# Optimization experiments

Hardware: AMD Instinct MI355X
Metric: run time of the kernel (lower is better)

Reference implementation:

```python
import jax, jax.numpy as jnp
import numpy as np

B, T, C = 2, 4096, 1024
H = 16
D = C // H  # head_dim = 64


def setup_inputs() -> dict:
    key = jax.random.key(0)
    k1, k2, k3 = jax.random.split(key, 3)
    x = jax.random.normal(k1, (B, T, C), dtype=jnp.float32)
    W_qkv = jax.random.normal(k2, (3 * C, C), dtype=jnp.float32) * (1.0 / np.sqrt(C))
    W_out = jax.random.normal(k3, (C, C), dtype=jnp.float32) * (1.0 / np.sqrt(C))
    return {"x": x, "W_qkv": W_qkv, "W_out": W_out}


def reference(x, W_qkv, W_out):
    b, t, c = x.shape
    # qkv projection: torch Linear y = x @ W.T  -> (B,T,3C)
    qkv = jnp.einsum('btc,fc->btf', x, W_qkv)
    qkv = qkv.reshape(b, t, 3, H, D)
    q, k, v = qkv[:, :, 0], qkv[:, :, 1], qkv[:, :, 2]  # (B,T,H,D)
    q = q.transpose(0, 2, 1, 3)  # (B,H,T,D)
    k = k.transpose(0, 2, 1, 3)
    v = v.transpose(0, 2, 1, 3)
    scale = 1.0 / np.sqrt(D).astype(np.float32)
    att = jnp.einsum('bhqd,bhkd->bhqk', q, k) * scale  # (B,H,T,T)
    causal = jnp.tril(jnp.ones((t, t), dtype=bool))
    att = jnp.where(causal[None, None], att, jnp.float32(-jnp.inf))
    att = jax.nn.softmax(att, axis=-1)
    # dropout p=0.0 -> identity
    out = jnp.einsum('bhqk,bhkd->bhqd', att, v)  # (B,H,T,D)
    out = out.transpose(0, 2, 1, 3).reshape(b, t, c)
    return jnp.einsum('btc,oc->bto', out, W_out)
```

## Files before the change

### kernel.cpp

```cpp
#include <hip/hip_runtime.h>

constexpr int Bn = 2;
constexpr int Tn = 4096;
constexpr int Cn = 1024;
constexpr int Hn = 16;
constexpr int Dn = 64;

typedef __bf16 bf16x8 __attribute__((ext_vector_type(8)));
typedef float f32x4 __attribute__((ext_vector_type(4)));
typedef unsigned short u16x8 __attribute__((ext_vector_type(8)));

__device__ __forceinline__ unsigned short f2bf(float f) {
  unsigned int u = __float_as_uint(f);
  u += 0x7FFF + ((u >> 16) & 1);
  return (unsigned short)(u >> 16);
}

__device__ __forceinline__ bf16x8 ld_bf8(const unsigned short* p) {
  return __builtin_bit_cast(bf16x8, *(const u16x8*)p);
}

__global__ void cvt_kernel(const float* __restrict__ in, unsigned short* __restrict__ out, int n4) {
  int i = blockIdx.x * blockDim.x + threadIdx.x;
  if (i >= n4) return;
  float4 v = ((const float4*)in)[i];
  ushort4 o;
  o.x = f2bf(v.x); o.y = f2bf(v.y); o.z = f2bf(v.z); o.w = f2bf(v.w);
  ((ushort4*)out)[i] = o;
}

template<int OUT_BF16>
__global__ __launch_bounds__(256) void gemm_bt(const unsigned short* __restrict__ A,
                                               const unsigned short* __restrict__ Bm,
                                               void* __restrict__ Cout,
                                               int M, int N, int K) {
  __shared__ __align__(16) unsigned short As[128][64];
  __shared__ __align__(16) unsigned short Bs[128][64];
  const int tid  = threadIdx.x;
  const int wave = tid >> 6;
  const int lane = tid & 63;
  const int wr   = (wave >> 1) * 64;
  const int wc   = (wave & 1) * 64;
  const int lrow = lane & 15;
  const int lk8  = (lane >> 4) << 3;
  const int row0 = blockIdx.y * 128;
  const int col0 = blockIdx.x * 128;

  f32x4 acc[4][4];
  #pragma unroll
  for (int i = 0; i < 4; ++i)
    #pragma unroll
    for (int j = 0; j < 4; ++j)
      acc[i][j] = (f32x4){0.f, 0.f, 0.f, 0.f};

  for (int k0 = 0; k0 < K; k0 += 64) {
    const unsigned short* Ag = A  + (size_t)row0 * K + k0;
    const unsigned short* Bg = Bm + (size_t)col0 * K + k0;
    #pragma unroll
    for (int i = 0; i < 4; ++i) {
      int flat = (i * 256 + tid) * 8;
      int r = flat >> 6, c = flat & 63;
      __builtin_amdgcn_global_load_lds((const __attribute__((address_space(1))) void*)(Ag + (size_t)r * K + c),
                                       (__attribute__((address_space(3))) void*)(&As[r][c]), 16, 0, 0);
    }
    #pragma unroll
    for (int i = 0; i < 4; ++i) {
      int flat = (i * 256 + tid) * 8;
      int r = flat >> 6, c = flat & 63;
      __builtin_amdgcn_global_load_lds((const __attribute__((address_space(1))) void*)(Bg + (size_t)r * K + c),
                                       (__attribute__((address_space(3))) void*)(&Bs[r][c]), 16, 0, 0);
    }
    __syncthreads();

    #pragma unroll
    for (int ks = 0; ks < 2; ++ks) {
      bf16x8 af[4], bfr[4];
      #pragma unroll
      for (int i = 0; i < 4; ++i) af[i]  = ld_bf8(&As[wr + i * 16 + lrow][ks * 32 + lk8]);
      #pragma unroll
      for (int j = 0; j < 4; ++j) bfr[j] = ld_bf8(&Bs[wc + j * 16 + lrow][ks * 32 + lk8]);
      #pragma unroll
      for (int i = 0; i < 4; ++i)
        #pragma unroll
        for (int j = 0; j < 4; ++j)
          acc[i][j] = __builtin_amdgcn_mfma_f32_16x16x32_bf16(af[i], bfr[j], acc[i][j], 0, 0, 0);
    }
    __syncthreads();
  }

  const int rg = (lane >> 4) * 4;
  const int cl = lane & 15;
  #pragma unroll
  for (int i = 0; i < 4; ++i)
    #pragma unroll
    for (int j = 0; j < 4; ++j)
      #pragma unroll
      for (int rr = 0; rr < 4; ++rr) {
        int gm = row0 + wr + i * 16 + rg + rr;
        int gn = col0 + wc + j * 16 + cl;
        float v = acc[i][j][rr];
        if (OUT_BF16) ((unsigned short*)Cout)[(size_t)gm * N + gn] = f2bf(v);
        else          ((float*)Cout)[(size_t)gm * N + gn] = v;
      }
}

__global__ __launch_bounds__(256) void vtrans_kernel(const unsigned short* __restrict__ qkv,
                                                     unsigned short* __restrict__ vT) {
  __shared__ __align__(16) unsigned short L[64 * 64];
  const int tid = threadIdx.x;
  const int t0  = blockIdx.x * 64;
  const int bh  = blockIdx.y;
  const int b   = bh >> 4;
  const int h   = bh & 15;
  const unsigned short* src = qkv + (size_t)b * Tn * (3 * Cn) + 2 * Cn + h * Dn;

  #pragma unroll
  for (int i = 0; i < 2; ++i) {
    int flat = i * 256 + tid;
    int t = flat >> 3, c = flat & 7;
    int cs = c ^ ((t >> 3) & 7);
    __builtin_amdgcn_global_load_lds(
        (const __attribute__((address_space(1))) void*)(src + (size_t)(t0 + t) * (3 * Cn) + cs * 8),
        (__attribute__((address_space(3))) void*)(&L[flat * 8]), 16, 0, 0);
  }
  __syncthreads();

  #pragma unroll
  for (int i = 0; i < 2; ++i) {
    int flat = i * 256 + tid;
    int d = flat >> 3, tc = flat & 7;
    u16x8 o;
    #pragma unroll
    for (int j = 0; j < 8; ++j) {
      int t = tc * 8 + j;
      o[j] = L[t * 64 + (((d >> 3) ^ ((t >> 3) & 7)) << 3) + (d & 7)];
    }
    *(u16x8*)(vT + ((size_t)bh * 64 + d) * Tn + t0 + tc * 8) = o;
  }
}

__global__ __launch_bounds__(256) void attn_kernel(const unsigned short* __restrict__ qkv,
                                                   const unsigned short* __restrict__ vT,
                                                   unsigned short* __restrict__ outb) {
  __shared__ __align__(16) unsigned short Ks[2][4096];
  __shared__ __align__(16) unsigned short Vs[2][4096];
  __shared__ __align__(16) unsigned short Ps[4][1024];

  const int tid  = threadIdx.x;
  const int wave = tid >> 6;
  const int lane = tid & 63;
  const int cl   = lane & 15;
  const int g    = lane >> 4;
  const int lk8  = g << 3;
  const int rg   = g * 4;

  const int orig = blockIdx.y * gridDim.x + blockIdx.x;
  const int cid  = (orig & 7) * 256 + (orig >> 3);
  const int qt   = (63 - (cid & 63)) * 64;
  const int bh   = cid >> 6;
  const int b    = bh >> 4;
  const int h    = bh & 15;

  const unsigned short* qb  = qkv + (size_t)b * Tn * (3 * Cn) + h * Dn;
  const unsigned short* kb  = qb + Cn;
  const unsigned short* vtb = vT + (size_t)bh * Dn * Tn;

  bf16x8 qf[2];
  {
    const unsigned short* qr = qb + (size_t)(qt + wave * 16 + cl) * (3 * Cn) + lk8;
    qf[0] = ld_bf8(qr);
    qf[1] = ld_bf8(qr + 32);
    #pragma unroll
    for (int j = 0; j < 8; ++j) {
      qf[0][j] = qf[0][j] * (__bf16)0.125f;
      qf[1][j] = qf[1][j] * (__bf16)0.125f;
    }
  }

  f32x4 oacc[4];
  #pragma unroll
  for (int n = 0; n < 4; ++n) oacc[n] = (f32x4){0.f, 0.f, 0.f, 0.f};
  float mrun[4] = {-1e30f, -1e30f, -1e30f, -1e30f};
  float lrun[4] = {0.f, 0.f, 0.f, 0.f};

  #pragma unroll
  for (int i = 0; i < 2; ++i) {
    const int flat = i * 256 + tid;
    const int r    = flat >> 3;
    const int cg   = flat & 7;
    const int sw   = cg ^ (r & 7);
    __builtin_amdgcn_global_load_lds(
        (const __attribute__((address_space(1))) void*)(kb + (size_t)r * (3 * Cn) + sw * 8),
        (__attribute__((address_space(3))) void*)(&Ks[0][flat * 8]), 16, 0, 0);
    __builtin_amdgcn_global_load_lds(
        (const __attribute__((address_space(1))) void*)(vtb + (size_t)r * Tn + sw * 8),
        (__attribute__((address_space(3))) void*)(&Vs[0][flat * 8]), 16, 0, 0);
  }
  __syncthreads();

  const int nkv = qt / 64 + 1;
  for (int kt = 0; kt < nkv; ++kt) {
    const int kv0 = kt * 64;
    const int cur = kt & 1;
    const int nb  = cur ^ 1;
    const bool pre = (kt + 1 < nkv);

    if (pre) {
      const int kv1 = kv0 + 64;
      #pragma unroll
      for (int i = 0; i < 2; ++i) {
        const int flat = i * 256 + tid;
        const int r    = flat >> 3;
        const int cg   = flat & 7;
        const int sw   = cg ^ (r & 7);
        __builtin_amdgcn_global_load_lds(
            (const __attribute__((address_space(1))) void*)(kb + (size_t)(kv1 + r) * (3 * Cn) + sw * 8),
            (__attribute__((address_space(3))) void*)(&Ks[nb][flat * 8]), 16, 0, 0);
        __builtin_amdgcn_global_load_lds(
            (const __attribute__((address_space(1))) void*)(vtb + (size_t)r * Tn + kv1 + sw * 8),
            (__attribute__((address_space(3))) void*)(&Vs[nb][flat * 8]), 16, 0, 0);
      }
    }

    f32x4 s[4];
    #pragma unroll
    for (int n = 0; n < 4; ++n) s[n] = (f32x4){0.f, 0.f, 0.f, 0.f};
    __builtin_amdgcn_s_setprio(1);
    #pragma unroll
    for (int n = 0; n < 4; ++n)
      #pragma unroll
      for (int ks = 0; ks < 2; ++ks) {
        bf16x8 kf = ld_bf8(&Ks[cur][(n * 16 + cl) * 64 + (((ks * 4 + g) ^ (cl & 7)) << 3)]);
        s[n] = __builtin_amdgcn_mfma_f32_16x16x32_bf16(qf[ks], kf, s[n], 0, 0, 0);
      }
    __builtin_amdgcn_s_setprio(0);

    const bool diag = (kv0 == qt);
    if (diag) {
      #pragma unroll
      for (int n = 0; n < 4; ++n)
        #pragma unroll
        for (int rr = 0; rr < 4; ++rr) {
          int ql = wave * 16 + rg + rr;
          int kl = n * 16 + cl;
          if (kl > ql) s[n][rr] = -1e30f;
        }
    }

    #pragma unroll
    for (int rr = 0; rr < 4; ++rr) {
      float mx = fmaxf(fmaxf(s[0][rr], s[1][rr]), fmaxf(s[2][rr], s[3][rr]));
      mx = fmaxf(mx, __shfl_xor(mx, 1));
      mx = fmaxf(mx, __shfl_xor(mx, 2));
      mx = fmaxf(mx, __shfl_xor(mx, 4));
      mx = fmaxf(mx, __shfl_xor(mx, 8));
      float mnew  = fmaxf(mrun[rr], mx);
      float alpha = __expf(mrun[rr] - mnew);
      mrun[rr] = mnew;
      float sum = 0.f;
      #pragma unroll
      for (int n = 0; n < 4; ++n) {
        float p = __expf(s[n][rr] - mnew);
        s[n][rr] = p;
        sum += p;
      }
      sum += __shfl_xor(sum, 1);
      sum += __shfl_xor(sum, 2);
      sum += __shfl_xor(sum, 4);
      sum += __shfl_xor(sum, 8);
      lrun[rr] = lrun[rr] * alpha + sum;
      #pragma unroll
      for (int n = 0; n < 4; ++n) oacc[n][rr] *= alpha;
    }

    #pragma unroll
    for (int n = 0; n < 4; ++n)
      #pragma unroll
      for (int rr = 0; rr < 4; ++rr) {
        const int row  = rg + rr;
        const int slot = n * 2 + (cl >> 3);
        Ps[wave][row * 64 + ((slot ^ (row & 7)) << 3) + (cl & 7)] = f2bf(s[n][rr]);
      }

    #pragma unroll
    for (int ks = 0; ks < 2; ++ks) {
      bf16x8 pa = ld_bf8(&Ps[wave][cl * 64 + (((ks * 4 + g) ^ (cl & 7)) << 3)]);
      __builtin_amdgcn_s_setprio(1);
      #pragma unroll
      for (int n = 0; n < 4; ++n) {
        bf16x8 vf = ld_bf8(&Vs[cur][(n * 16 + cl) * 64 + (((ks * 4 + g) ^ (cl & 7)) << 3)]);
        oacc[n] = __builtin_amdgcn_mfma_f32_16x16x32_bf16(pa, vf, oacc[n], 0, 0, 0);
      }
      __builtin_amdgcn_s_setprio(0);
    }

    __syncthreads();
  }

  #pragma unroll
  for (int rr = 0; rr < 4; ++rr) {
    float inv = 1.0f / lrun[rr];
    int t = qt + wave * 16 + rg + rr;
    size_t rowo = ((size_t)b * Tn + t) * Cn + h * Dn;
    #pragma unroll
    for (int n = 0; n < 4; ++n)
      outb[rowo + n * 16 + cl] = f2bf(oacc[n][rr] * inv);
  }
}

extern "C" void kernel_launch(void* const* d_in, const int* in_sizes, int n_in,
                              void* d_out, int out_size, void* d_ws, size_t ws_size,
                              hipStream_t stream) {
  const float* x    = (const float*)d_in[0];
  const float* Wqkv = (const float*)d_in[1];
  const float* Wout = (const float*)d_in[2];
  float* y = (float*)d_out;

  unsigned short* xb    = (unsigned short*)d_ws;
  unsigned short* wqkvb = xb    + (size_t)Bn * Tn * Cn;
  unsigned short* woutb = wqkvb + (size_t)3 * Cn * Cn;
  unsigned short* qkvb  = woutb + (size_t)Cn * Cn;
  unsigned short* attno = qkvb  + (size_t)Bn * Tn * 3 * Cn;

  const int M = Bn * Tn;

  {
    int n4 = (Bn * Tn * Cn) / 4;
    cvt_kernel<<<(n4 + 255) / 256, 256, 0, stream>>>(x, xb, n4);
  }
  {
    int n4 = (3 * Cn * Cn) / 4;
    cvt_kernel<<<(n4 + 255) / 256, 256, 0, stream>>>(Wqkv, wqkvb, n4);
  }
  {
    int n4 = (Cn * Cn) / 4;
    cvt_kernel<<<(n4 + 255) / 256, 256, 0, stream>>>(Wout, woutb, n4);
  }

  gemm_bt<1><<<dim3(3 * Cn / 128, M / 128), 256, 0, stream>>>(xb, wqkvb, qkvb, M, 3 * Cn, Cn);

  unsigned short* vT = xb;
  vtrans_kernel<<<dim3(Tn / 64, Bn * Hn), 256, 0, stream>>>(qkvb, vT);

  attn_kernel<<<dim3(Tn / 64, Bn * Hn), 256, 0, stream>>>(qkvb, vT, attno);

  gemm_bt<0><<<dim3(Cn / 128, M / 128), 256, 0, stream>>>(attno, woutb, y, M, Cn, Cn);

  (void)in_sizes; (void)n_in; (void)out_size; (void)ws_size;
}
```

Measured before the change: 448.6 us.

## Skip softmax rescale when max unchanged, defer row-sum reduce, swizzle GEMM tiles

New measurement: 413.0 us. 1.09x faster.

```diff
diff --git a/kernel.cpp b/kernel.cpp
--- a/kernel.cpp
+++ b/kernel.cpp
@@ -14,6 +14,10 @@
   unsigned int u = __float_as_uint(f);
   u += 0x7FFF + ((u >> 16) & 1);
   return (unsigned short)(u >> 16);
+}
+
+__device__ __forceinline__ unsigned short f2bf_hw(float f) {
+  return __builtin_bit_cast(unsigned short, (__bf16)f);
 }
 
 __device__ __forceinline__ bf16x8 ld_bf8(const unsigned short* p) {
@@ -43,8 +47,13 @@
   const int wc   = (wave & 1) * 64;
   const int lrow = lane & 15;
   const int lk8  = (lane >> 4) << 3;
-  const int row0 = blockIdx.y * 128;
-  const int col0 = blockIdx.x * 128;
+
+  const int nbx  = gridDim.x;
+  const int nwg  = nbx * gridDim.y;
+  const int orig = blockIdx.y * nbx + blockIdx.x;
+  const int cid  = (orig & 7) * (nwg >> 3) + (orig >> 3);
+  const int row0 = (cid / nbx) * 128;
+  const int col0 = (cid % nbx) * 128;
 
   f32x4 acc[4][4];
   #pragma unroll
@@ -247,6 +256,7 @@
         }
     }
 
+    float pmax[4];
     #pragma unroll
     for (int rr = 0; rr < 4; ++rr) {
       float mx = fmaxf(fmaxf(s[0][rr], s[1][rr]), fmaxf(s[2][rr], s[3][rr]));
@@ -254,23 +264,39 @@
       mx = fmaxf(mx, __shfl_xor(mx, 2));
       mx = fmaxf(mx, __shfl_xor(mx, 4));
       mx = fmaxf(mx, __shfl_xor(mx, 8));
-      float mnew  = fmaxf(mrun[rr], mx);
-      float alpha = __expf(mrun[rr] - mnew);
-      mrun[rr] = mnew;
-      float sum = 0.f;
-      #pragma unroll
-      for (int n = 0; n < 4; ++n) {
-        float p = __expf(s[n][rr] - mnew);
-        s[n][rr] = p;
-        sum += p;
-      }
-      sum += __shfl_xor(sum, 1);
-      sum += __shfl_xor(sum, 2);
-      sum += __shfl_xor(sum, 4);
-      sum += __shfl_xor(sum, 8);
-      lrun[rr] = lrun[rr] * alpha + sum;
-      #pragma unroll
-      for (int n = 0; n < 4; ++n) oacc[n][rr] *= alpha;
+      pmax[rr] = mx;
+    }
+    const bool need = (pmax[0] > mrun[0]) || (pmax[1] > mrun[1]) ||
+                      (pmax[2] > mrun[2]) || (pmax[3] > mrun[3]);
+    if (__any(need)) {
+      #pragma unroll
+      for (int rr = 0; rr < 4; ++rr) {
+        float mnew  = fmaxf(mrun[rr], pmax[rr]);
+        float alpha = __expf(mrun[rr] - mnew);
+        mrun[rr] = mnew;
+        float psum = 0.f;
+        #pragma unroll
+        for (int n = 0; n < 4; ++n) {
+          float p = __expf(s[n][rr] - mnew);
+          s[n][rr] = p;
+          psum += p;
+        }
+        lrun[rr] = lrun[rr] * alpha + psum;
+        #pragma unroll
+        for (int n = 0; n < 4; ++n) oacc[n][rr] *= alpha;
+      }
+    } else {
+      #pragma unroll
+      for (int rr = 0; rr < 4; ++rr) {
+        float psum = 0.f;
+        #pragma unroll
+        for (int n = 0; n < 4; ++n) {
+          float p = __expf(s[n][rr] - mrun[rr]);
+          s[n][rr] = p;
+          psum += p;
+        }
+        lrun[rr] += psum;
+      }
     }
 
     #pragma unroll
@@ -279,7 +305,7 @@
       for (int rr = 0; rr < 4; ++rr) {
         const int row  = rg + rr;
         const int slot = n * 2 + (cl >> 3);
-        Ps[wave][row * 64 + ((slot ^ (row & 7)) << 3) + (cl & 7)] = f2bf(s[n][rr]);
+        Ps[wave][row * 64 + ((slot ^ (row & 7)) << 3) + (cl & 7)] = f2bf_hw(s[n][rr]);
       }
 
     #pragma unroll
@@ -297,6 +323,13 @@
     __syncthreads();
   }
 
+  #pragma unroll
+  for (int rr = 0; rr < 4; ++rr) {
+    lrun[rr] += __shfl_xor(lrun[rr], 1);
+    lrun[rr] += __shfl_xor(lrun[rr], 2);
+    lrun[rr] += __shfl_xor(lrun[rr], 4);
+    lrun[rr] += __shfl_xor(lrun[rr], 8);
+  }
   #pragma unroll
   for (int rr = 0; rr < 4; ++rr) {
     float inv = 1.0f / lrun[rr];
@@ -304,7 +337,7 @@
     size_t rowo = ((size_t)b * Tn + t) * Cn + h * Dn;
     #pragma unroll
     for (int n = 0; n < 4; ++n)
-      outb[rowo + n * 16 + cl] = f2bf(oacc[n][rr] * inv);
+      outb[rowo + n * 16 + cl] = f2bf_hw(oacc[n][rr] * inv);
   }
 }
 
```
